# Kernel tuning notes

Measured on AMD Instinct MI355X. Metric: run time of the kernel, lower is better.

## Reference

```python
import jax, jax.numpy as jnp
import numpy as np

N, F, K = 2048, 256, 4
E = 65536

def setup_inputs() -> dict:
    key = jax.random.key(0)
    ks = jax.random.split(key, 8)
    batch_x = jax.random.normal(ks[0], (N, F), dtype=jnp.float32)
    # eigen-matrix of a normalized Laplacian is diagonal in practice, but the
    # original code treats it as a dense [N,N] operand; we mimic a diagonal
    # eigenvalue matrix (eigenvalues in [0,2]) -- math is identical either way.
    lam_diag = 2.0 * jax.random.uniform(ks[1], (N,), dtype=jnp.float32)
    batch_lam = jnp.diag(lam_diag)
    batch_U = jax.random.normal(ks[2], (N, N), dtype=jnp.float32) / jnp.sqrt(jnp.float32(N))
    # init.uniform_(a, 0, 2) / (b, 0, 2) / (c, -1, 1); keep a-b bounded away from 0
    a_list = 1.0 + jax.random.uniform(ks[3], (K,), dtype=jnp.float32)        # [1,2)
    b_list = 0.9 * jax.random.uniform(ks[4], (K,), dtype=jnp.float32)       # [0,0.9)
    c_list = 2.0 * jax.random.uniform(ks[5], (K,), dtype=jnp.float32) - 1.0  # [-1,1)
    residual_alpha = jnp.ones((1,), dtype=jnp.float32)
    edge_index = jax.random.randint(ks[6], (2, E), 0, N, dtype=jnp.int64)
    return {"batch_x": batch_x, "batch_lam": batch_lam, "batch_U": batch_U,
            "a_list": a_list, "b_list": b_list, "c_list": c_list,
            "residual_alpha": residual_alpha, "edge_index": edge_index}

def reference(batch_x, batch_lam, batch_U, a_list, b_list, c_list, residual_alpha, edge_index):
    n = batch_lam.shape[0]
    I = jnp.eye(n, dtype=batch_lam.dtype)
    out = residual_alpha * batch_x  # residual added at hop 0 in original
    for i in range(a_list.shape[0]):
        # filter_rep = (a_i*I - Lam) @ (Lam - b_i*I), then relu
        rep = (a_list[i] * I - batch_lam) @ (batch_lam - b_list[i] * I)
        rep = jax.nn.relu(rep)
        scale = c_list[i] / ((a_list[i] - b_list[i]) * (a_list[i] - b_list[i]) / 4.0)
        filt = scale * (batch_U @ (rep @ (batch_U.T @ batch_x)))
        out = out + filt
    return out
```

## Files before the change

### kernel.cpp

```cpp
#include <hip/hip_runtime.h>
#include <type_traits>

typedef unsigned short u16;
typedef __attribute__((ext_vector_type(8))) short short8;
typedef __attribute__((ext_vector_type(4))) float floatx4;

__device__ __forceinline__ u16 f2u(float f) {
  unsigned int x = __float_as_uint(f);
  x += 0x7fff + ((x >> 16) & 1);
  return (u16)(x >> 16);
}

__device__ __forceinline__ void async16(const void* g, void* l) {
  __builtin_amdgcn_global_load_lds(
      (const __attribute__((address_space(1))) unsigned int*)g,
      (__attribute__((address_space(3))) unsigned int*)l, 16, 0, 0);
}

__global__ __launch_bounds__(256) void prep_kernel(
    const float* __restrict__ U, const float* __restrict__ x,
    u16* __restrict__ Ut, u16* __restrict__ Ubf, u16* __restrict__ xT,
    int N, int F) {
  __shared__ __attribute__((aligned(16))) float tile[64][65];
  int bb = blockIdx.x;
  int t = threadIdx.x;

  const float* in;
  u16 *outT, *outC;
  int R, C, c0, r0;
  if (bb < 1024) {
    in = U; outT = Ut; outC = Ubf; R = N; C = N;
    c0 = (bb & 31) * 64; r0 = (bb >> 5) * 64;
  } else {
    int b2 = bb - 1024;
    in = x; outT = xT; outC = nullptr; R = N; C = F;
    c0 = (b2 & 3) * 64; r0 = (b2 >> 2) * 64;
  }

#pragma unroll
  for (int p = 0; p < 4; ++p) {
    int e = p * 256 + t;
    int row = e >> 4, col = (e & 15) * 4;
    float4 v = *(const float4*)(in + (size_t)(r0 + row) * C + c0 + col);
    tile[row][col] = v.x;
    tile[row][col + 1] = v.y;
    tile[row][col + 2] = v.z;
    tile[row][col + 3] = v.w;
    if (outC) {
      union { uint2 u; u16 s[4]; } pk;
      pk.s[0] = f2u(v.x); pk.s[1] = f2u(v.y);
      pk.s[2] = f2u(v.z); pk.s[3] = f2u(v.w);
      *(uint2*)(outC + (size_t)(r0 + row) * C + c0 + col) = pk.u;
    }
  }
  __syncthreads();
#pragma unroll
  for (int p = 0; p < 2; ++p) {
    int e = p * 256 + t;
    int orow = e >> 3, oc = (e & 7) * 8;
    union { uint4 v; u16 s[8]; } tmp;
#pragma unroll
    for (int i = 0; i < 8; ++i) tmp.s[i] = f2u(tile[oc + i][orow]);
    *(uint4*)(outT + (size_t)(c0 + orow) * R + r0 + oc) = tmp.v;
  }
}

template <bool WIDE_N, bool SCALE_D, bool RESIDUAL, typename CT>
__global__ __launch_bounds__(256) void gemm32(
    const u16* __restrict__ A, const u16* __restrict__ B, CT* __restrict__ C,
    int M, int NN, int K, const float* __restrict__ lam,
    const float* __restrict__ pa, const float* __restrict__ pb,
    const float* __restrict__ pc, const float* __restrict__ resid,
    const float* __restrict__ alpha_p) {
  __shared__ __attribute__((aligned(16))) u16 lA[2 * 8192];
  __shared__ __attribute__((aligned(16))) u16 lB[2 * 8192];
  const int b = blockIdx.x;
  int m0, n0;
  if (WIDE_N) {
    m0 = ((b >> 3) & 7) * 32;
    n0 = ((b & 7) * 8 + (b >> 6)) * 32;
  } else {
    m0 = ((b & 7) * 8 + (b >> 6)) * 32;
    n0 = ((b >> 3) & 7) * 32;
  }
  const int t = threadIdx.x;
  const int wave = t >> 6, lane = t & 63;
  const int q = lane >> 4, l15 = lane & 15;

  const int within = t & 127, st0 = t >> 7;
  const int srow = within >> 2;
  const int schunk = (within & 3) ^ ((srow >> 1) & 3);
  const u16* gA = A + (size_t)(m0 + srow) * K + schunk * 8;
  const u16* gB = B + (size_t)(n0 + srow) * K + schunk * 8;
  char* lAc = (char*)lA;
  char* lBc = (char*)lB;

  const int NM = K >> 8;

  auto issue = [&](int i, int buf) {
    int k0 = i * 256;
#pragma unroll
    for (int p = 0; p < 4; ++p) {
      int st = 2 * p + st0;
      async16(gA + k0 + st * 32, lAc + buf * 16384 + p * 4096 + t * 16);
      async16(gB + k0 + st * 32, lBc + buf * 16384 + p * 4096 + t * 16);
    }
  };

  floatx4 acc[2][2];
#pragma unroll
  for (int m = 0; m < 2; ++m)
#pragma unroll
    for (int n = 0; n < 2; ++n) acc[m][n] = (floatx4){0.f, 0.f, 0.f, 0.f};

  const int ksw = (q ^ ((l15 >> 1) & 3)) * 8;

  issue(0, 0);
  for (int i = 0; i < NM; ++i) {
    const int buf = i & 1;
    __syncthreads();
    if (i + 1 < NM) issue(i + 1, buf ^ 1);
    const u16* lAb = lA + buf * 8192;
    const u16* lBb = lB + buf * 8192;
#pragma unroll
    for (int ss = 0; ss < 2; ++ss) {
      const int st = 2 * wave + ss;
      const u16* As = lAb + st * 1024;
      const u16* Bs = lBb + st * 1024;
      short8 af[2], bf[2];
#pragma unroll
      for (int m = 0; m < 2; ++m)
        af[m] = *(const short8*)&As[(m * 16 + l15) * 32 + ksw];
#pragma unroll
      for (int n = 0; n < 2; ++n)
        bf[n] = *(const short8*)&Bs[(n * 16 + l15) * 32 + ksw];
#pragma unroll
      for (int m = 0; m < 2; ++m)
#pragma unroll
        for (int n = 0; n < 2; ++n)
          acc[m][n] =
              __builtin_amdgcn_mfma_f32_16x16x32_bf16(af[m], bf[n], acc[m][n], 0, 0, 0);
    }
  }

  __syncthreads();
  float* red = (float*)lA;
#pragma unroll
  for (int m = 0; m < 2; ++m)
#pragma unroll
    for (int n = 0; n < 2; ++n)
#pragma unroll
      for (int r = 0; r < 4; ++r)
        red[wave * 1024 + (m * 16 + q * 4 + r) * 32 + n * 16 + l15] = acc[m][n][r];
  __syncthreads();

  const int col = t & 31;
  float ds = 1.f;
  if (SCALE_D) {
    const int ac = n0 + col;
    float lv = lam[(size_t)ac * NN + ac];
    float dacc = 0.f;
#pragma unroll
    for (int i = 0; i < 4; ++i) {
      float ai = pa[i], bi = pb[i], ci = pc[i];
      float rep = (ai - lv) * (lv - bi);
      rep = rep > 0.f ? rep : 0.f;
      dacc += ci * 4.f / ((ai - bi) * (ai - bi)) * rep;
    }
    ds = dacc;
  }
  float alpha = 0.f;
  if (RESIDUAL) alpha = alpha_p[0];
#pragma unroll
  for (int p = 0; p < 4; ++p) {
    const int row = (t >> 5) + p * 8;
    const int e = row * 32 + col;
    float v = red[e] + red[1024 + e] + red[2048 + e] + red[3072 + e];
    if (SCALE_D) v *= ds;
    size_t idx = (size_t)(m0 + row) * NN + (n0 + col);
    if (RESIDUAL) v += alpha * resid[idx];
    if constexpr (std::is_same<CT, u16>::value)
      C[idx] = f2u(v);
    else
      C[idx] = v;
  }
}

extern "C" void kernel_launch(void* const* d_in, const int* in_sizes, int n_in,
                              void* d_out, int out_size, void* d_ws,
                              size_t ws_size, hipStream_t stream) {
  const int N = 2048, F = 256;
  const float* x = (const float*)d_in[0];
  const float* lam = (const float*)d_in[1];
  const float* U = (const float*)d_in[2];
  const float* a = (const float*)d_in[3];
  const float* b = (const float*)d_in[4];
  const float* c = (const float*)d_in[5];
  const float* alpha = (const float*)d_in[6];

  char* ws = (char*)d_ws;
  u16* xT = (u16*)ws;
  u16* Ut = (u16*)(ws + (1 << 20));
  u16* Ubf = (u16*)(ws + (9 << 20));
  u16* zT = (u16*)(ws + (17 << 20));

  prep_kernel<<<1152, 256, 0, stream>>>(U, x, Ut, Ubf, xT, N, F);
  gemm32<true, true, false, u16><<<512, 256, 0, stream>>>(
      xT, Ut, zT, F, N, N, lam, a, b, c, nullptr, nullptr);
  gemm32<false, false, true, float><<<512, 256, 0, stream>>>(
      Ubf, zT, (float*)d_out, N, F, N, nullptr, nullptr, nullptr, nullptr,
      x, alpha);
}
```

Measured before the change: 107.1 us.

## Fuse prep and both GEMMs into one cooperative kernel with grid syncs

Merges the transpose/convert prep and the two bf16 GEMM stages into a single persistent cooperative launch of 512 blocks, with grid-wide barriers between phases, and falls back to the three separate launches if the cooperative launch fails. The aim is to remove kernel launch gaps and inter-kernel drain/fill between the stages. In exchange it caps parallelism at 512 resident blocks, so each block loops over prep tiles. It also adds grid.sync overhead and needs all 512 blocks of 64KB LDS to be co-resident.

```diff
diff --git a/kernel.cpp b/kernel.cpp
--- a/kernel.cpp
+++ b/kernel.cpp
@@ -1,5 +1,8 @@
 #include <hip/hip_runtime.h>
+#include <hip/hip_cooperative_groups.h>
 #include <type_traits>
+
+namespace cg = cooperative_groups;
 
 typedef unsigned short u16;
 typedef __attribute__((ext_vector_type(8))) short short8;
@@ -17,12 +20,12 @@
       (__attribute__((address_space(3))) unsigned int*)l, 16, 0, 0);
 }
 
-__global__ __launch_bounds__(256) void prep_kernel(
-    const float* __restrict__ U, const float* __restrict__ x,
+__device__ __forceinline__ void prep_tile(
+    int bb, const float* __restrict__ U, const float* __restrict__ x,
     u16* __restrict__ Ut, u16* __restrict__ Ubf, u16* __restrict__ xT,
-    int N, int F) {
-  __shared__ __attribute__((aligned(16))) float tile[64][65];
-  int bb = blockIdx.x;
+    char* sm) {
+  const int N = 2048, F = 256;
+  float (*tile)[65] = (float (*)[65])sm;
   int t = threadIdx.x;
 
   const float* in;
@@ -63,17 +66,18 @@
     for (int i = 0; i < 8; ++i) tmp.s[i] = f2u(tile[oc + i][orow]);
     *(uint4*)(outT + (size_t)(c0 + orow) * R + r0 + oc) = tmp.v;
   }
+  __syncthreads();
 }
 
 template <bool WIDE_N, bool SCALE_D, bool RESIDUAL, typename CT>
-__global__ __launch_bounds__(256) void gemm32(
-    const u16* __restrict__ A, const u16* __restrict__ B, CT* __restrict__ C,
-    int M, int NN, int K, const float* __restrict__ lam,
+__device__ __forceinline__ void gemm_phase(
+    char* sm, const u16* __restrict__ A, const u16* __restrict__ B,
+    CT* __restrict__ C, int NN, int K, const float* __restrict__ lam,
     const float* __restrict__ pa, const float* __restrict__ pb,
     const float* __restrict__ pc, const float* __restrict__ resid,
     const float* __restrict__ alpha_p) {
-  __shared__ __attribute__((aligned(16))) u16 lA[2 * 8192];
-  __shared__ __attribute__((aligned(16))) u16 lB[2 * 8192];
+  u16* lA = (u16*)sm;
+  u16* lB = (u16*)(sm + 32768);
   const int b = blockIdx.x;
   int m0, n0;
   if (WIDE_N) {
@@ -138,8 +142,8 @@
       for (int m = 0; m < 2; ++m)
 #pragma unroll
         for (int n = 0; n < 2; ++n)
-          acc[m][n] =
-              __builtin_amdgcn_mfma_f32_16x16x32_bf16(af[m], bf[n], acc[m][n], 0, 0, 0);
+          acc[m][n] = __builtin_amdgcn_mfma_f32_16x16x32_bf16(af[m], bf[n],
+                                                              acc[m][n], 0, 0, 0);
     }
   }
 
@@ -184,6 +188,46 @@
     else
       C[idx] = v;
   }
+  __syncthreads();
+}
+
+__global__ __launch_bounds__(256) void fused_all(
+    const float* __restrict__ x, const float* __restrict__ lam,
+    const float* __restrict__ U, const float* __restrict__ a,
+    const float* __restrict__ b, const float* __restrict__ c,
+    const float* __restrict__ alpha, u16* __restrict__ xT,
+    u16* __restrict__ Ut, u16* __restrict__ Ubf, u16* __restrict__ zT,
+    float* __restrict__ out) {
+  __shared__ __attribute__((aligned(16))) char sm[65536];
+  cg::grid_group grid = cg::this_grid();
+
+  for (int job = blockIdx.x; job < 1152; job += gridDim.x)
+    prep_tile(job, U, x, Ut, Ubf, xT, sm);
+  grid.sync();
+  gemm_phase<true, true, false, u16>(sm, xT, Ut, zT, 2048, 2048, lam, a, b, c,
+                                     nullptr, nullptr);
+  grid.sync();
+  gemm_phase<false, false, true, float>(sm, Ubf, zT, out, 256, 2048, nullptr,
+                                        nullptr, nullptr, nullptr, x, alpha);
+}
+
+__global__ __launch_bounds__(256) void prep_kernel(
+    const float* __restrict__ U, const float* __restrict__ x,
+    u16* __restrict__ Ut, u16* __restrict__ Ubf, u16* __restrict__ xT,
+    int N, int F) {
+  __shared__ __attribute__((aligned(16))) char sm[65536];
+  prep_tile(blockIdx.x, U, x, Ut, Ubf, xT, sm);
+}
+
+template <bool WIDE_N, bool SCALE_D, bool RESIDUAL, typename CT>
+__global__ __launch_bounds__(256) void gemm32(
+    const u16* __restrict__ A, const u16* __restrict__ B, CT* __restrict__ C,
+    int NN, int K, const float* __restrict__ lam, const float* __restrict__ pa,
+    const float* __restrict__ pb, const float* __restrict__ pc,
+    const float* __restrict__ resid, const float* __restrict__ alpha_p) {
+  __shared__ __attribute__((aligned(16))) char sm[65536];
+  gemm_phase<WIDE_N, SCALE_D, RESIDUAL, CT>(sm, A, B, C, NN, K, lam, pa, pb, pc,
+                                            resid, alpha_p);
 }
 
 extern "C" void kernel_launch(void* const* d_in, const int* in_sizes, int n_in,
@@ -203,11 +247,18 @@
   u16* Ut = (u16*)(ws + (1 << 20));
   u16* Ubf = (u16*)(ws + (9 << 20));
   u16* zT = (u16*)(ws + (17 << 20));
-
-  prep_kernel<<<1152, 256, 0, stream>>>(U, x, Ut, Ubf, xT, N, F);
-  gemm32<true, true, false, u16><<<512, 256, 0, stream>>>(
-      xT, Ut, zT, F, N, N, lam, a, b, c, nullptr, nullptr);
-  gemm32<false, false, true, float><<<512, 256, 0, stream>>>(
-      Ubf, zT, (float*)d_out, N, F, N, nullptr, nullptr, nullptr, nullptr,
-      x, alpha);
-}
+  float* outp = (float*)d_out;
+
+  void* args[] = {(void*)&x,  (void*)&lam, (void*)&U,   (void*)&a,
+                  (void*)&b,  (void*)&c,   (void*)&alpha, (void*)&xT,
+                  (void*)&Ut, (void*)&Ubf, (void*)&zT,  (void*)&outp};
+  hipError_t err = hipLaunchCooperativeKernel((const void*)fused_all, dim3(512),
+                                              dim3(256), args, 0, stream);
+  if (err != hipSuccess) {
+    prep_kernel<<<1152, 256, 0, stream>>>(U, x, Ut, Ubf, xT, N, F);
+    gemm32<true, true, false, u16><<<512, 256, 0, stream>>>(
+        xT, Ut, zT, N, N, lam, a, b, c, nullptr, nullptr);
+    gemm32<false, false, true, float><<<512, 256, 0, stream>>>(
+        Ubf, zT, outp, F, N, nullptr, nullptr, nullptr, nullptr, x, alpha);
+  }
+}
```

Measured after the change: 233.4 us. 2.18x slower.

## Convert U to bf16 inside the second GEMM instead of the prep kernel

Applied to the files above, without the earlier changes.

The prep kernel no longer writes a row-major bf16 copy of U. The second GEMM now reads fp32 U straight from global memory into registers, converts it to bf16, and stores it into LDS through a software pipeline two stages deep, while B still arrives through async global-to-LDS loads. This removes an 8 MB bf16 write and its later read-back. In exchange the GEMM reads 16 MB of fp32 instead of 8 MB of bf16 and carries more register pressure and conversion work in its main loop.

```diff
diff --git a/kernel.cpp b/kernel.cpp
--- a/kernel.cpp
+++ b/kernel.cpp
@@ -1,5 +1,4 @@
 #include <hip/hip_runtime.h>
-#include <type_traits>
 
 typedef unsigned short u16;
 typedef __attribute__((ext_vector_type(8))) short short8;
@@ -19,21 +18,20 @@
 
 __global__ __launch_bounds__(256) void prep_kernel(
     const float* __restrict__ U, const float* __restrict__ x,
-    u16* __restrict__ Ut, u16* __restrict__ Ubf, u16* __restrict__ xT,
-    int N, int F) {
+    u16* __restrict__ Ut, u16* __restrict__ xT, int N, int F) {
   __shared__ __attribute__((aligned(16))) float tile[64][65];
   int bb = blockIdx.x;
   int t = threadIdx.x;
 
   const float* in;
-  u16 *outT, *outC;
+  u16* outT;
   int R, C, c0, r0;
   if (bb < 1024) {
-    in = U; outT = Ut; outC = Ubf; R = N; C = N;
+    in = U; outT = Ut; R = N; C = N;
     c0 = (bb & 31) * 64; r0 = (bb >> 5) * 64;
   } else {
     int b2 = bb - 1024;
-    in = x; outT = xT; outC = nullptr; R = N; C = F;
+    in = x; outT = xT; R = N; C = F;
     c0 = (b2 & 3) * 64; r0 = (b2 >> 2) * 64;
   }
 
@@ -46,12 +44,6 @@
     tile[row][col + 1] = v.y;
     tile[row][col + 2] = v.z;
     tile[row][col + 3] = v.w;
-    if (outC) {
-      union { uint2 u; u16 s[4]; } pk;
-      pk.s[0] = f2u(v.x); pk.s[1] = f2u(v.y);
-      pk.s[2] = f2u(v.z); pk.s[3] = f2u(v.w);
-      *(uint2*)(outC + (size_t)(r0 + row) * C + c0 + col) = pk.u;
-    }
   }
   __syncthreads();
 #pragma unroll
@@ -65,24 +57,15 @@
   }
 }
 
-template <bool WIDE_N, bool SCALE_D, bool RESIDUAL, typename CT>
-__global__ __launch_bounds__(256) void gemm32(
-    const u16* __restrict__ A, const u16* __restrict__ B, CT* __restrict__ C,
-    int M, int NN, int K, const float* __restrict__ lam,
-    const float* __restrict__ pa, const float* __restrict__ pb,
-    const float* __restrict__ pc, const float* __restrict__ resid,
-    const float* __restrict__ alpha_p) {
+__global__ __launch_bounds__(256) void gemm1(
+    const u16* __restrict__ A, const u16* __restrict__ B, u16* __restrict__ C,
+    int NN, int K, const float* __restrict__ lam, const float* __restrict__ pa,
+    const float* __restrict__ pb, const float* __restrict__ pc) {
   __shared__ __attribute__((aligned(16))) u16 lA[2 * 8192];
   __shared__ __attribute__((aligned(16))) u16 lB[2 * 8192];
   const int b = blockIdx.x;
-  int m0, n0;
-  if (WIDE_N) {
-    m0 = ((b >> 3) & 7) * 32;
-    n0 = ((b & 7) * 8 + (b >> 6)) * 32;
-  } else {
-    m0 = ((b & 7) * 8 + (b >> 6)) * 32;
-    n0 = ((b >> 3) & 7) * 32;
-  }
+  const int m0 = ((b >> 3) & 7) * 32;
+  const int n0 = ((b & 7) * 8 + (b >> 6)) * 32;
   const int t = threadIdx.x;
   const int wave = t >> 6, lane = t & 63;
   const int q = lane >> 4, l15 = lane & 15;
@@ -138,8 +121,8 @@
       for (int m = 0; m < 2; ++m)
 #pragma unroll
         for (int n = 0; n < 2; ++n)
-          acc[m][n] =
-              __builtin_amdgcn_mfma_f32_16x16x32_bf16(af[m], bf[n], acc[m][n], 0, 0, 0);
+          acc[m][n] = __builtin_amdgcn_mfma_f32_16x16x32_bf16(af[m], bf[n],
+                                                              acc[m][n], 0, 0, 0);
     }
   }
 
@@ -155,34 +138,140 @@
   __syncthreads();
 
   const int col = t & 31;
-  float ds = 1.f;
-  if (SCALE_D) {
-    const int ac = n0 + col;
-    float lv = lam[(size_t)ac * NN + ac];
-    float dacc = 0.f;
-#pragma unroll
-    for (int i = 0; i < 4; ++i) {
-      float ai = pa[i], bi = pb[i], ci = pc[i];
-      float rep = (ai - lv) * (lv - bi);
-      rep = rep > 0.f ? rep : 0.f;
-      dacc += ci * 4.f / ((ai - bi) * (ai - bi)) * rep;
-    }
-    ds = dacc;
-  }
-  float alpha = 0.f;
-  if (RESIDUAL) alpha = alpha_p[0];
+  const int ac = n0 + col;
+  float lv = lam[(size_t)ac * NN + ac];
+  float ds = 0.f;
+#pragma unroll
+  for (int i = 0; i < 4; ++i) {
+    float ai = pa[i], bi = pb[i], ci = pc[i];
+    float rep = (ai - lv) * (lv - bi);
+    rep = rep > 0.f ? rep : 0.f;
+    ds += ci * 4.f / ((ai - bi) * (ai - bi)) * rep;
+  }
+#pragma unroll
+  for (int p = 0; p < 4; ++p) {
+    const int row = (t >> 5) + p * 8;
+    const int e = row * 32 + col;
+    float v = (red[e] + red[1024 + e] + red[2048 + e] + red[3072 + e]) * ds;
+    C[(size_t)(m0 + row) * NN + ac] = f2u(v);
+  }
+}
+
+__global__ __launch_bounds__(256) void gemm2_uf32(
+    const float* __restrict__ A, const u16* __restrict__ B,
+    float* __restrict__ C, const float* __restrict__ resid,
+    const float* __restrict__ alpha_p) {
+  const int K = 2048, NN = 256, NM = 8;
+  __shared__ __attribute__((aligned(16))) u16 lA[2 * 8192];
+  __shared__ __attribute__((aligned(16))) u16 lB[2 * 8192];
+  const int b = blockIdx.x;
+  const int m0 = ((b & 7) * 8 + (b >> 6)) * 32;
+  const int n0 = ((b >> 3) & 7) * 32;
+  const int t = threadIdx.x;
+  const int wave = t >> 6, lane = t & 63;
+  const int q = lane >> 4, l15 = lane & 15;
+
+  const int within = t & 127, st0 = t >> 7;
+  const int srow = within >> 2;
+  const int schunk = (within & 3) ^ ((srow >> 1) & 3);
+  const float* gA = A + (size_t)(m0 + srow) * K + schunk * 8;
+  const u16* gB = B + (size_t)(n0 + srow) * K + schunk * 8;
+  char* lAc = (char*)lA;
+  char* lBc = (char*)lB;
+
+  auto issueB = [&](int i, int buf) {
+    int k0 = i * 256;
+#pragma unroll
+    for (int p = 0; p < 4; ++p)
+      async16(gB + k0 + (2 * p + st0) * 32, lBc + buf * 16384 + p * 4096 + t * 16);
+  };
+
+  float4 ra[2][8];
+  auto loadA = [&](int i, int s) {
+    int k0 = i * 256;
+#pragma unroll
+    for (int p = 0; p < 4; ++p) {
+      const float* src = gA + k0 + (2 * p + st0) * 32;
+      ra[s][2 * p] = *(const float4*)src;
+      ra[s][2 * p + 1] = *(const float4*)(src + 4);
+    }
+  };
+  auto writeA = [&](int s, int buf) {
+#pragma unroll
+    for (int p = 0; p < 4; ++p) {
+      union { uint4 v; u16 u[8]; } pk;
+      float4 lo = ra[s][2 * p], hi = ra[s][2 * p + 1];
+      pk.u[0] = f2u(lo.x); pk.u[1] = f2u(lo.y);
+      pk.u[2] = f2u(lo.z); pk.u[3] = f2u(lo.w);
+      pk.u[4] = f2u(hi.x); pk.u[5] = f2u(hi.y);
+      pk.u[6] = f2u(hi.z); pk.u[7] = f2u(hi.w);
+      *(uint4*)(lAc + buf * 16384 + p * 4096 + t * 16) = pk.v;
+    }
+  };
+
+  floatx4 acc[2][2];
+#pragma unroll
+  for (int m = 0; m < 2; ++m)
+#pragma unroll
+    for (int n = 0; n < 2; ++n) acc[m][n] = (floatx4){0.f, 0.f, 0.f, 0.f};
+
+  const int ksw = (q ^ ((l15 >> 1) & 3)) * 8;
+
+  loadA(0, 0);
+  issueB(0, 0);
+  loadA(1, 1);
+  writeA(0, 0);
+
+#pragma unroll
+  for (int i = 0; i < NM; ++i) {
+    const int buf = i & 1;
+    __syncthreads();
+    if (i + 1 < NM) issueB(i + 1, buf ^ 1);
+    if (i + 2 < NM) loadA(i + 2, i & 1);
+    const u16* lAb = lA + buf * 8192;
+    const u16* lBb = lB + buf * 8192;
+#pragma unroll
+    for (int ss = 0; ss < 2; ++ss) {
+      const int st = 2 * wave + ss;
+      const u16* As = lAb + st * 1024;
+      const u16* Bs = lBb + st * 1024;
+      short8 af[2], bf[2];
+#pragma unroll
+      for (int m = 0; m < 2; ++m)
+        af[m] = *(const short8*)&As[(m * 16 + l15) * 32 + ksw];
+#pragma unroll
+      for (int n = 0; n < 2; ++n)
+        bf[n] = *(const short8*)&Bs[(n * 16 + l15) * 32 + ksw];
+#pragma unroll
+      for (int m = 0; m < 2; ++m)
+#pragma unroll
+        for (int n = 0; n < 2; ++n)
+          acc[m][n] = __builtin_amdgcn_mfma_f32_16x16x32_bf16(af[m], bf[n],
+                                                              acc[m][n], 0, 0, 0);
+    }
+    if (i + 1 < NM) writeA((i + 1) & 1, buf ^ 1);
+  }
+
+  __syncthreads();
+  float* red = (float*)lA;
+#pragma unroll
+  for (int m = 0; m < 2; ++m)
+#pragma unroll
+    for (int n = 0; n < 2; ++n)
+#pragma unroll
+      for (int r = 0; r < 4; ++r)
+        red[wave * 1024 + (m * 16 + q * 4 + r) * 32 + n * 16 + l15] = acc[m][n][r];
+  __syncthreads();
+
+  const int col = t & 31;
+  const float alpha = alpha_p[0];
 #pragma unroll
   for (int p = 0; p < 4; ++p) {
     const int row = (t >> 5) + p * 8;
     const int e = row * 32 + col;
     float v = red[e] + red[1024 + e] + red[2048 + e] + red[3072 + e];
-    if (SCALE_D) v *= ds;
     size_t idx = (size_t)(m0 + row) * NN + (n0 + col);
-    if (RESIDUAL) v += alpha * resid[idx];
-    if constexpr (std::is_same<CT, u16>::value)
-      C[idx] = f2u(v);
-    else
-      C[idx] = v;
+    C[idx] = v + alpha * resid[idx];
   }
 }
 
@@ -201,13 +290,9 @@
   char* ws = (char*)d_ws;
   u16* xT = (u16*)ws;
   u16* Ut = (u16*)(ws + (1 << 20));
-  u16* Ubf = (u16*)(ws + (9 << 20));
-  u16* zT = (u16*)(ws + (17 << 20));
-
-  prep_kernel<<<1152, 256, 0, stream>>>(U, x, Ut, Ubf, xT, N, F);
-  gemm32<true, true, false, u16><<<512, 256, 0, stream>>>(
-      xT, Ut, zT, F, N, N, lam, a, b, c, nullptr, nullptr);
-  gemm32<false, false, true, float><<<512, 256, 0, stream>>>(
-      Ubf, zT, (float*)d_out, N, F, N, nullptr, nullptr, nullptr, nullptr,
-      x, alpha);
-}
+  u16* zT = (u16*)(ws + (9 << 20));
+
+  prep_kernel<<<1152, 256, 0, stream>>>(U, x, Ut, xT, N, F);
+  gemm1<<<512, 256, 0, stream>>>(xT, Ut, zT, N, N, lam, a, b, c);
+  gemm2_uf32<<<512, 256, 0, stream>>>(U, zT, (float*)d_out, x, alpha);
+}
```

Result: slower. 112.0 us (+4.5%).
